# Kernel optimization log

Hardware: AMD Instinct MI355X
Metric: run time of the kernel (lower is better)

## Reference

```python
import jax, jax.numpy as jnp
import numpy as np

N_HEADS = 8

def lstm_step(x, h, c, W_ih, W_hh, b_ih, b_hh):
    # torch LSTMCell: gate order i, f, g, o
    gates = x @ W_ih.T + b_ih + h @ W_hh.T + b_hh
    i, f, g, o = jnp.split(gates, 4, axis=-1)
    c = jax.nn.sigmoid(f) * c + jax.nn.sigmoid(i) * jnp.tanh(g)
    h = jax.nn.sigmoid(o) * jnp.tanh(c)
    return h, c

def mha(query, key, value, attn_mask, Wq, bq, Wk, bk, Wv, bv, Wo, bo):
    # query [B,1,H], key/value [B,N,H], attn_mask [B,1,N] (True = masked)
    B, N, H = key.shape
    dh = H // N_HEADS
    q = (query @ Wq.T + bq).reshape(B, 1, N_HEADS, dh)
    k = (key @ Wk.T + bk).reshape(B, N, N_HEADS, dh)
    v = (value @ Wv.T + bv).reshape(B, N, N_HEADS, dh)
    scores = jnp.einsum('bqhd,bnhd->bhqn', q, k) / jnp.sqrt(jnp.asarray(dh, q.dtype))
    scores = jnp.where(attn_mask[:, None, :, :], jnp.asarray(-1e9, scores.dtype), scores)
    attn = jax.nn.softmax(scores, axis=-1)
    out = jnp.einsum('bhqn,bnhd->bqhd', attn, v).reshape(B, 1, H)
    return out @ Wo.T + bo

def setup_inputs() -> dict:
    B, S, V, E, G, HI, N = 32, 128, 32000, 512, 1024, 512, 16
    ks = jax.random.split(jax.random.key(0), 24)
    s = 0.05
    inp = {}
    inp['entity_feature'] = jax.random.normal(ks[0], (B, HI), jnp.float32)
    inp['neighbor_feature'] = jax.random.normal(ks[1], (B, N, HI), jnp.float32)
    inp['neighbor_num'] = jax.random.randint(ks[2], (B,), 1, N + 1)
    inp['img_feature'] = jax.random.normal(ks[3], (B, HI), jnp.float32)
    inp['target_sent'] = jax.random.randint(ks[4], (B, S), 0, V)
    inp['target_sent_len'] = jax.random.randint(ks[5], (B,), 1, S)
    emb = jax.random.normal(ks[6], (V, E), jnp.float32) * s
    inp['embedding'] = emb.at[0].set(0.0)  # padding_idx = 0
    inp['W_ih'] = jax.random.normal(ks[7], (4 * G, E), jnp.float32) * s
    inp['W_hh'] = jax.random.normal(ks[8], (4 * G, G), jnp.float32) * s
    inp['b_ih'] = jnp.zeros((4 * G,), jnp.float32)
    inp['b_hh'] = jnp.zeros((4 * G,), jnp.float32)
    inp['W_img'] = jax.random.normal(ks[9], (E, 3 * HI), jnp.float32) * s
    inp['b_img'] = jnp.zeros((E,), jnp.float32)
    inp['W_out'] = jax.random.normal(ks[10], (V, G), jnp.float32) * s
    inp['b_out'] = jnp.zeros((V,), jnp.float32)
    inp['Wq'] = jax.random.normal(ks[11], (HI, HI), jnp.float32) * s
    inp['bq'] = jnp.zeros((HI,), jnp.float32)
    inp['Wk'] = jax.random.normal(ks[12], (HI, HI), jnp.float32) * s
    inp['bk'] = jnp.zeros((HI,), jnp.float32)
    inp['Wv'] = jax.random.normal(ks[13], (HI, HI), jnp.float32) * s
    inp['bv'] = jnp.zeros((HI,), jnp.float32)
    inp['Wo'] = jax.random.normal(ks[14], (HI, HI), jnp.float32) * s
    inp['bo'] = jnp.zeros((HI,), jnp.float32)
    return inp

def reference(entity_feature, neighbor_feature, neighbor_num, img_feature,
              target_sent, target_sent_len, embedding,
              W_ih, W_hh, b_ih, b_hh, W_img, b_img, W_out, b_out,
              Wq, bq, Wk, bk, Wv, bv, Wo, bo):
    B = img_feature.shape[0]
    G = W_hh.shape[1]
    N = neighbor_feature.shape[1]
    # generate_final_feature: masked MHA of entity over neighbors
    mask = (neighbor_num[:, None] <= jnp.arange(N)[None, :])[:, None, :]  # [B,1,N]
    attn_out = mha(entity_feature[:, None, :], neighbor_feature, neighbor_feature, mask,
                   Wq, bq, Wk, bk, Wv, bv, Wo, bo).reshape(B, -1)
    final_feature = jnp.concatenate([entity_feature, attn_out, img_feature], axis=-1)
    img_embed = jnp.tanh(final_feature @ W_img.T + b_img)  # [B,E]
    z = jnp.zeros((B, G), img_embed.dtype)
    h, c = lstm_step(img_embed, z, z, W_ih, W_hh, b_ih, b_hh)
    # teacher forcing over t = 0..S-2 (dropout is identity in eval mode)
    x = embedding[target_sent[:, :-1]]  # [B, S-1, E]
    def step(carry, xt):
        h, c = carry
        h, c = lstm_step(xt, h, c, W_ih, W_hh, b_ih, b_hh)
        return (h, c), h @ W_out.T + b_out
    _, logits = jax.lax.scan(step, (h, c), jnp.swapaxes(x, 0, 1))  # [S-1,B,V]
    pred_words_probs = jnp.swapaxes(logits, 0, 1)  # [B, S-1, V]
    return pred_words_probs, target_sent, target_sent_len
```

## Files before the change

### kernel.cpp

```cpp
#include <hip/hip_runtime.h>
#include <math.h>

typedef short v8s __attribute__((ext_vector_type(8)));
typedef float v4f __attribute__((ext_vector_type(4)));

#define B_   32
#define S_   128
#define V_   32000
#define E_   512
#define G_   1024
#define HI_  512
#define NN_  16
#define NH_  8
#define DH_  64
#define TSTEPS 127
#define LOGN  4064000L
#define SCAN_BLOCKS 128

__device__ __forceinline__ short to_bf16(float x) {
  union { float f; unsigned u; } a; a.f = x;
  unsigned r = (a.u + 0x7FFFu + ((a.u >> 16) & 1u)) >> 16;
  return (short)r;
}
__device__ __forceinline__ float sigf(float x) { return 1.f / (1.f + expf(-x)); }

__device__ __forceinline__ void load_lds16(const void* g, void* l) {
  __builtin_amdgcn_global_load_lds((const __attribute__((address_space(1))) void*)g,
                                   (__attribute__((address_space(3))) void*)l, 16, 0, 0);
}

__global__ void prep_kernel(const float* __restrict__ Wih, const float* __restrict__ Whh,
                            const float* __restrict__ Wout, const float* __restrict__ bih,
                            const float* __restrict__ bhh, const int* __restrict__ sent,
                            const int* __restrict__ slen,
                            short* __restrict__ Wih_b, short* __restrict__ Whh_b,
                            short* __restrict__ Wout_b, float* __restrict__ bsum,
                            float* __restrict__ outTail, unsigned* __restrict__ flags) {
  const long nWo = 32768000L, nWh = 4194304L, nWi = 2097152L;
  const long NT = nWo + nWh + nWi + 4096 + 4096 + 32 + 128;
  long stride = (long)gridDim.x * blockDim.x;
  for (long i = (long)blockIdx.x * blockDim.x + threadIdx.x; i < NT; i += stride) {
    if (i < nWo) { Wout_b[i] = to_bf16(Wout[i]); continue; }
    long j = i - nWo;
    if (j < nWh) { Whh_b[j] = to_bf16(Whh[j]); continue; }
    j -= nWh;
    if (j < nWi) { Wih_b[j] = to_bf16(Wih[j]); continue; }
    j -= nWi;
    if (j < 4096) { bsum[j] = bih[j] + bhh[j]; continue; }
    j -= 4096;
    if (j < 4096) { outTail[j] = (float)sent[j]; continue; }
    j -= 4096;
    if (j < 32) { outTail[4096 + j] = (float)slen[j]; continue; }
    j -= 32;
    flags[j] = 0u;
  }
}

__global__ void dotk(const float* __restrict__ X, const float* __restrict__ W,
                     const float* __restrict__ bias, float* __restrict__ out,
                     int M, int N, int K, int act) {
  int o = blockIdx.x * 256 + threadIdx.x;
  if (o >= M * N) return;
  int m = o / N, n = o % N;
  const float4* x4 = (const float4*)(X + (long)m * K);
  const float4* w4 = (const float4*)(W + (long)n * K);
  float s = 0.f;
  int k4 = K >> 2;
  for (int k = 0; k < k4; ++k) {
    float4 a = x4[k], b = w4[k];
    s += a.x * b.x + a.y * b.y + a.z * b.z + a.w * b.w;
  }
  s += bias[n];
  if (act) s = tanhf(s);
  out[o] = s;
}

__global__ void attnk(const float* __restrict__ q, const float* __restrict__ k,
                      const float* __restrict__ v, const int* __restrict__ nnum,
                      float* __restrict__ ctx) {
  __shared__ float sc[NN_], at[NN_];
  int blk = blockIdx.x;
  int b = blk >> 3, h = blk & 7;
  int t = threadIdx.x;
  if (t < NN_) {
    const float* qp = q + b * HI_ + h * DH_;
    const float* kp = k + (long)(b * NN_ + t) * HI_ + h * DH_;
    float s = 0.f;
    for (int d = 0; d < DH_; ++d) s += qp[d] * kp[d];
    s *= 0.125f;
    if (t >= nnum[b]) s = -1e9f;
    sc[t] = s;
  }
  __syncthreads();
  if (t == 0) {
    float mx = sc[0];
    for (int n = 1; n < NN_; ++n) mx = fmaxf(mx, sc[n]);
    float sum = 0.f;
    for (int n = 0; n < NN_; ++n) { float e = expf(sc[n] - mx); at[n] = e; sum += e; }
    float inv = 1.f / sum;
    for (int n = 0; n < NN_; ++n) at[n] *= inv;
  }
  __syncthreads();
  float acc = 0.f;
  for (int n = 0; n < NN_; ++n)
    acc += at[n] * v[(long)(b * NN_ + n) * HI_ + h * DH_ + t];
  ctx[b * HI_ + h * DH_ + t] = acc;
}

__global__ void concatk(const float* __restrict__ ent, const float* __restrict__ ao,
                        const float* __restrict__ img, float* __restrict__ ff) {
  int i = blockIdx.x * 256 + threadIdx.x;
  if (i >= B_ * 3 * HI_) return;
  int b = i / (3 * HI_), j = i % (3 * HI_);
  float vv;
  if (j < HI_) vv = ent[b * HI_ + j];
  else if (j < 2 * HI_) vv = ao[b * HI_ + j - HI_];
  else vv = img[b * HI_ + j - 2 * HI_];
  ff[i] = vv;
}

__global__ void lstm0(const float* __restrict__ g0, float* __restrict__ c0,
                      short* __restrict__ HB) {
  int i = blockIdx.x * 256 + threadIdx.x;
  if (i >= B_ * G_) return;
  int b = i >> 10, u = i & 1023;
  const float* gr = g0 + (long)b * 4096;
  float ig = gr[u], gg = gr[2048 + u], og = gr[3072 + u];
  float c = sigf(ig) * tanhf(gg);
  float h = sigf(og) * tanhf(c);
  c0[i] = c;
  HB[i] = to_bf16(h);
}

__global__ void gatherk(const float* __restrict__ emb, const int* __restrict__ sent,
                        short* __restrict__ Xemb) {
  int i = blockIdx.x * 256 + threadIdx.x;
  if (i >= 4096 * 512) return;
  int mrow = i >> 9, e = i & 511;
  int t = mrow >> 5, b = mrow & 31;
  float vv = 0.f;
  if (t < TSTEPS) { int w = sent[b * S_ + t]; vv = emb[(long)w * E_ + e]; }
  Xemb[i] = to_bf16(vv);
}

__global__ __launch_bounds__(256) void gemm_bt(const short* __restrict__ A,
                                               const short* __restrict__ Bm,
                                               const float* __restrict__ bias,
                                               float* __restrict__ C,
                                               int M, int N, int K, int mode) {
  __shared__ short As[128 * 32];
  __shared__ short Bs[128 * 32];
  const int tid = threadIdx.x;
  const int lane = tid & 63, wave = tid >> 6;
  const int n0 = blockIdx.x * 128, m0 = blockIdx.y * 128;
  const int l15 = lane & 15, quad = lane >> 4;
  const int mhalf = wave & 1, nhalf = wave >> 1;
  const int srow = lane >> 2;
  const int sseg = (lane & 3) * 8;
  v4f acc[4][4];
#pragma unroll
  for (int i = 0; i < 4; i++)
#pragma unroll
    for (int j = 0; j < 4; j++) acc[i][j] = (v4f){0.f, 0.f, 0.f, 0.f};
  const int kiters = K >> 5;
  for (int kt = 0; kt < kiters; ++kt) {
    const int k0 = kt * 32;
#pragma unroll
    for (int c = 0; c < 2; ++c) {
      const int chunk = wave * 2 + c;
      const int row = chunk * 16 + srow;
      load_lds16(A + (long)(m0 + row) * K + k0 + sseg, &As[chunk * 512]);
      load_lds16(Bm + (long)(n0 + row) * K + k0 + sseg, &Bs[chunk * 512]);
    }
    __syncthreads();
    v8s af[4], wf[4];
#pragma unroll
    for (int i = 0; i < 4; i++) af[i] = *(const v8s*)&As[(mhalf * 64 + i * 16 + l15) * 32 + quad * 8];
#pragma unroll
    for (int j = 0; j < 4; j++) wf[j] = *(const v8s*)&Bs[(nhalf * 64 + j * 16 + l15) * 32 + quad * 8];
#pragma unroll
    for (int i = 0; i < 4; i++)
#pragma unroll
      for (int j = 0; j < 4; j++)
        acc[i][j] = __builtin_amdgcn_mfma_f32_16x16x32_bf16(af[i], wf[j], acc[i][j], 0, 0, 0);
    __syncthreads();
  }
#pragma unroll
  for (int i = 0; i < 4; i++) {
    const int mb = m0 + mhalf * 64 + i * 16 + quad * 4;
#pragma unroll
    for (int j = 0; j < 4; j++) {
      const int nc = n0 + nhalf * 64 + j * 16 + l15;
      const float bv = bias[nc];
#pragma unroll
      for (int r = 0; r < 4; r++) {
        const int m = mb + r;
        float vv = acc[i][j][r] + bv;
        if (mode == 0) {
          C[(long)m * N + nc] = vv;
        } else if (m >= 32) {
          const int b = m & 31, t = (m >> 5) - 1;
          C[(long)b * LOGN + (long)t * V_ + nc] = vv;
        }
      }
    }
  }
}

__global__ __launch_bounds__(256) void lstm_scan(const float* __restrict__ Xg,
                                                 const short* __restrict__ Whh_b,
                                                 const float* __restrict__ c0,
                                                 short* __restrict__ HB,
                                                 unsigned* __restrict__ flags) {
  __shared__ short Wl[32 * 1032];
  __shared__ short Hl[32 * 1032];
  __shared__ float gl[32 * 33];
  __shared__ float cl[256];
  const int tid = threadIdx.x, nb = blockIdx.x;
  const int lane = tid & 63, wave = tid >> 6;
  const int l15 = lane & 15, quad = lane >> 4;
  const int mt = wave & 1, nt = wave >> 1;

  for (int cid = tid; cid < 4096; cid += 256) {
    int lrow = cid >> 7;
    int koff = (cid & 127) * 8;
    int u = lrow >> 2, g = lrow & 3;
    const short* src = Whh_b + (long)(g * 1024 + nb * 8 + u) * 1024 + koff;
    *(v8s*)&Wl[lrow * 1032 + koff] = *(const v8s*)src;
  }
  const int eu = tid >> 5, eb = tid & 31, gu = nb * 8 + eu;
  cl[tid] = c0[eb * 1024 + gu];
  __syncthreads();

  float x0, x1, x2, x3;
  {
    const float* xr = Xg + (long)eb * 4096 + gu;
    x0 = xr[0]; x1 = xr[1024]; x2 = xr[2048]; x3 = xr[3072];
  }

  for (int tt = 0; tt < TSTEPS; ++tt) {
    {
      const short* hsrc = HB + (long)tt * 32 * 1024;
#pragma unroll
      for (int it = 0; it < 16; ++it) {
        int cid = it * 256 + tid;
        int row = cid >> 7;
        int koff = (cid & 127) * 8;
        *(v8s*)&Hl[row * 1032 + koff] = *(const v8s*)(hsrc + cid * 8);
      }
    }
    __syncthreads();
    v4f acc0 = (v4f){0.f, 0.f, 0.f, 0.f};
    v4f acc1 = (v4f){0.f, 0.f, 0.f, 0.f};
    {
      const short* aP = &Hl[(mt * 16 + l15) * 1032 + quad * 8];
      const short* wP = &Wl[(nt * 16 + l15) * 1032 + quad * 8];
#pragma unroll
      for (int kk = 0; kk < 32; kk += 2) {
        v8s a0 = *(const v8s*)(aP + kk * 32);
        v8s w0 = *(const v8s*)(wP + kk * 32);
        v8s a1 = *(const v8s*)(aP + (kk + 1) * 32);
        v8s w1 = *(const v8s*)(wP + (kk + 1) * 32);
        acc0 = __builtin_amdgcn_mfma_f32_16x16x32_bf16(a0, w0, acc0, 0, 0, 0);
        acc1 = __builtin_amdgcn_mfma_f32_16x16x32_bf16(a1, w1, acc1, 0, 0, 0);
      }
    }
#pragma unroll
    for (int r = 0; r < 4; ++r)
      gl[(nt * 16 + l15) * 33 + mt * 16 + quad * 4 + r] = acc0[r] + acc1[r];
    __syncthreads();
    float ig = gl[(eu * 4 + 0) * 33 + eb] + x0;
    float fg = gl[(eu * 4 + 1) * 33 + eb] + x1;
    float gg = gl[(eu * 4 + 2) * 33 + eb] + x2;
    float og = gl[(eu * 4 + 3) * 33 + eb] + x3;
    float c = sigf(fg) * cl[tid] + sigf(ig) * tanhf(gg);
    float h = sigf(og) * tanhf(c);
    cl[tid] = c;
    unsigned hb = (unsigned)(unsigned short)to_bf16(h);
    unsigned ob = (unsigned)__shfl((int)hb, lane ^ 32, 64);
    if ((lane & 32) == 0) {
      unsigned packed = hb | (ob << 16);
      unsigned* dst = (unsigned*)HB + ((long)(tt + 1) * 32 + eb) * 512 + nb * 4 + wave;
      __hip_atomic_store(dst, packed, __ATOMIC_RELAXED, __HIP_MEMORY_SCOPE_AGENT);
    }
    asm volatile("s_waitcnt vmcnt(0)" ::: "memory");
    __syncthreads();
    if (tt < TSTEPS - 1) {
      if (tid == 0)
        __hip_atomic_store(flags + nb, (unsigned)(tt + 1), __ATOMIC_RELAXED, __HIP_MEMORY_SCOPE_AGENT);
      {
        const float* xn = Xg + ((long)(tt + 1) * 32 + eb) * 4096 + gu;
        x0 = xn[0]; x1 = xn[1024]; x2 = xn[2048]; x3 = xn[3072];
      }
      if (tid < 64) {
        const unsigned long long* fp = (const unsigned long long*)flags + tid;
        const unsigned tgt = (unsigned)(tt + 1);
        for (;;) {
          unsigned long long v = __hip_atomic_load(fp, __ATOMIC_RELAXED, __HIP_MEMORY_SCOPE_AGENT);
          if ((unsigned)v >= tgt && (unsigned)(v >> 32) >= tgt) break;
          __builtin_amdgcn_s_sleep(2);
        }
      }
      __syncthreads();
    }
  }
}

extern "C" void kernel_launch(void* const* d_in, const int* in_sizes, int n_in,
                              void* d_out, int out_size, void* d_ws, size_t ws_size,
                              hipStream_t stream) {
  const float* ent  = (const float*)d_in[0];
  const float* nei  = (const float*)d_in[1];
  const int*   nnum = (const int*)d_in[2];
  const float* img  = (const float*)d_in[3];
  const int*   sent = (const int*)d_in[4];
  const int*   slen = (const int*)d_in[5];
  const float* emb  = (const float*)d_in[6];
  const float* Wih  = (const float*)d_in[7];
  const float* Whh  = (const float*)d_in[8];
  const float* bih  = (const float*)d_in[9];
  const float* bhh  = (const float*)d_in[10];
  const float* Wimg = (const float*)d_in[11];
  const float* bimg = (const float*)d_in[12];
  const float* Wout = (const float*)d_in[13];
  const float* bout = (const float*)d_in[14];
  const float* Wq = (const float*)d_in[15]; const float* bq = (const float*)d_in[16];
  const float* Wk = (const float*)d_in[17]; const float* bk = (const float*)d_in[18];
  const float* Wv = (const float*)d_in[19]; const float* bv = (const float*)d_in[20];
  const float* Wo = (const float*)d_in[21]; const float* bo = (const float*)d_in[22];
  float* out = (float*)d_out;

  char* ws = (char*)d_ws;
  short* Wout_b = (short*)(ws + 0L);
  short* Whh_b  = (short*)(ws + 65536000L);
  short* Wih_b  = (short*)(ws + 73924608L);
  float* bsum   = (float*)(ws + 78118912L);
  short* Xemb   = (short*)(ws + 78135296L);
  short* HB     = (short*)(ws + 82329600L);
  float* qbuf   = (float*)(ws + 90718208L);
  float* kbuf   = (float*)(ws + 90783744L);
  float* vbuf   = (float*)(ws + 91832320L);
  float* ctxb   = (float*)(ws + 92880896L);
  float* aob    = (float*)(ws + 92946432L);
  float* ffb    = (float*)(ws + 93011968L);
  float* ieb    = (float*)(ws + 93208576L);
  float* g0b    = (float*)(ws + 93274112L);
  float* c0b    = (float*)(ws + 93798400L);
  unsigned* flags = (unsigned*)(ws + 93929472L);
  float* Xg = out;
  float* outTail = out + (long)B_ * TSTEPS * V_;

  prep_kernel<<<16384, 256, 0, stream>>>(Wih, Whh, Wout, bih, bhh, sent, slen,
                                         Wih_b, Whh_b, Wout_b, bsum, outTail, flags);
  dotk<<<64, 256, 0, stream>>>(ent, Wq, bq, qbuf, 32, 512, 512, 0);
  dotk<<<1024, 256, 0, stream>>>(nei, Wk, bk, kbuf, 512, 512, 512, 0);
  dotk<<<1024, 256, 0, stream>>>(nei, Wv, bv, vbuf, 512, 512, 512, 0);
  attnk<<<256, 64, 0, stream>>>(qbuf, kbuf, vbuf, nnum, ctxb);
  dotk<<<64, 256, 0, stream>>>(ctxb, Wo, bo, aob, 32, 512, 512, 0);
  concatk<<<192, 256, 0, stream>>>(ent, aob, img, ffb);
  dotk<<<64, 256, 0, stream>>>(ffb, Wimg, bimg, ieb, 32, 512, 1536, 1);
  dotk<<<512, 256, 0, stream>>>(ieb, Wih, bsum, g0b, 32, 4096, 512, 0);
  lstm0<<<128, 256, 0, stream>>>(g0b, c0b, HB);
  gatherk<<<8192, 256, 0, stream>>>(emb, sent, Xemb);
  gemm_bt<<<dim3(32, 32), 256, 0, stream>>>(Xemb, Wih_b, bsum, Xg, 4096, 4096, 512, 0);
  lstm_scan<<<SCAN_BLOCKS, 256, 0, stream>>>(Xg, Whh_b, c0b, HB, flags);
  gemm_bt<<<dim3(250, 32), 256, 0, stream>>>(HB, Wout_b, bout, out, 4096, 32000, 1024, 1);
}
```

Baseline: 2.182 ms.

## Fuse vocab projection GEMM into LSTM scan as flag-gated worker blocks

The scan kernel now launches extra worker blocks that run the 4096x32000x1024 output GEMM tile by tile. Each worker spins on the per-block step flags until the hidden states its M-tile needs are published, so the projection overlaps the serial recurrence instead of running after it. The input-gate precompute is written into the output buffer in an interleaved layout, so each scan thread reads its four gates with one float4 load. Workers overwrite that scratch region only after the scan has consumed it. In exchange the GEMM gets half as many blocks, and correctness depends on all 256 blocks being co-resident and on the flag ordering.

```diff
diff --git a/kernel.cpp b/kernel.cpp
--- a/kernel.cpp
+++ b/kernel.cpp
@@ -16,6 +16,10 @@
 #define TSTEPS 127
 #define LOGN  4064000L
 #define SCAN_BLOCKS 128
+#define WORK_BLOCKS 128
+#define NTILES 250
+#define MTILES 32
+#define TOTTILES 8000
 
 __device__ __forceinline__ short to_bf16(float x) {
   union { float f; unsigned u; } a; a.f = x;
@@ -198,27 +202,132 @@
         float vv = acc[i][j][r] + bv;
         if (mode == 0) {
           C[(long)m * N + nc] = vv;
-        } else if (m >= 32) {
-          const int b = m & 31, t = (m >> 5) - 1;
-          C[(long)b * LOGN + (long)t * V_ + nc] = vv;
-        }
-      }
-    }
-  }
-}
-
-__global__ __launch_bounds__(256) void lstm_scan(const float* __restrict__ Xg,
-                                                 const short* __restrict__ Whh_b,
-                                                 const float* __restrict__ c0,
-                                                 short* __restrict__ HB,
-                                                 unsigned* __restrict__ flags) {
-  __shared__ short Wl[32 * 1032];
-  __shared__ short Hl[32 * 1032];
-  __shared__ float gl[32 * 33];
-  __shared__ float cl[256];
+        } else {
+          if (m < 4064) {
+            const int u = m >> 5, b = m & 31;
+            const int uu = nc & 1023, g = nc >> 10;
+            C[(long)b * LOGN + (long)u * 32000 + (uu >> 3) * 32 + (uu & 7) * 4 + g] = vv;
+          }
+        }
+      }
+    }
+  }
+}
+
+__global__ __launch_bounds__(256) void lstm_scan(const short* Whh_b,
+                                                 const float* c0,
+                                                 short* HB,
+                                                 unsigned* flags,
+                                                 const short* Wout_b,
+                                                 const float* bout,
+                                                 float* outb) {
+  __shared__ __align__(16) char smem[137344];
   const int tid = threadIdx.x, nb = blockIdx.x;
   const int lane = tid & 63, wave = tid >> 6;
   const int l15 = lane & 15, quad = lane >> 4;
+  const int mhalf = wave & 1, nhalf = wave >> 1;
+
+  if (nb >= SCAN_BLOCKS) {
+    const int wid = nb - SCAN_BLOCKS;
+    const int rsub = lane >> 3;
+    const int cswz = ((lane & 7) * 16) ^ (rsub << 4);
+    int lastm = -1;
+    for (int q = wid; q < TOTTILES; q += WORK_BLOCKS) {
+      const int mt_ = q / NTILES, nt_ = q % NTILES;
+      const int m0 = mt_ * 128, n0 = nt_ * 128;
+      if (mt_ != lastm) {
+        lastm = mt_;
+        unsigned tgt = (unsigned)(mt_ * 4 + 3);
+        if (tgt > 127u) tgt = 127u;
+        if (tid < 64) {
+          const unsigned long long* fp = (const unsigned long long*)flags + tid;
+          for (;;) {
+            unsigned long long vv = __hip_atomic_load(fp, __ATOMIC_RELAXED, __HIP_MEMORY_SCOPE_AGENT);
+            if ((unsigned)vv >= tgt && (unsigned)(vv >> 32) >= tgt) break;
+            __builtin_amdgcn_s_sleep(4);
+          }
+        }
+        asm volatile("" ::: "memory");
+        __syncthreads();
+      }
+      v4f acc[4][4];
+#pragma unroll
+      for (int i = 0; i < 4; i++)
+#pragma unroll
+        for (int j = 0; j < 4; j++) acc[i][j] = (v4f){0.f, 0.f, 0.f, 0.f};
+
+      auto wissue = [&](int s2) {
+        if (s2 < 16) {
+          const long k0b = (long)s2 * 128;
+          char* Ab = smem + (s2 & 3) * 32768;
+          char* Bb = Ab + 16384;
+#pragma unroll
+          for (int c = 0; c < 4; ++c) {
+            const int rowb = wave * 32 + c * 8;
+            load_lds16((const char*)HB + (long)(m0 + rowb + rsub) * 2048 + k0b + cswz,
+                       Ab + rowb * 128);
+            load_lds16((const char*)Wout_b + (long)(n0 + rowb + rsub) * 2048 + k0b + cswz,
+                       Bb + rowb * 128);
+          }
+        }
+      };
+      wissue(0); wissue(1); wissue(2);
+      for (int s = 0; s < 16; ++s) {
+        wissue(s + 3);
+        if (s <= 12)      asm volatile("s_waitcnt vmcnt(24)" ::: "memory");
+        else if (s == 13) asm volatile("s_waitcnt vmcnt(16)" ::: "memory");
+        else if (s == 14) asm volatile("s_waitcnt vmcnt(8)" ::: "memory");
+        else              asm volatile("s_waitcnt vmcnt(0)" ::: "memory");
+        __builtin_amdgcn_s_barrier();
+        const short* Ab = (const short*)(smem + (s & 3) * 32768);
+        const short* Bb = Ab + 8192;
+#pragma unroll
+        for (int kk = 0; kk < 2; ++kk) {
+          v8s af[4], bf[4];
+#pragma unroll
+          for (int i = 0; i < 4; ++i) {
+            const int row = mhalf * 64 + i * 16 + l15;
+            af[i] = *(const v8s*)(Ab + row * 64 + ((kk * 32 + quad * 8) ^ ((row & 7) << 3)));
+          }
+#pragma unroll
+          for (int j = 0; j < 4; ++j) {
+            const int row = nhalf * 64 + j * 16 + l15;
+            bf[j] = *(const v8s*)(Bb + row * 64 + ((kk * 32 + quad * 8) ^ ((row & 7) << 3)));
+          }
+#pragma unroll
+          for (int i = 0; i < 4; ++i)
+#pragma unroll
+            for (int j = 0; j < 4; ++j)
+              acc[i][j] = __builtin_amdgcn_mfma_f32_16x16x32_bf16(af[i], bf[j], acc[i][j], 0, 0, 0);
+        }
+        asm volatile("" ::: "memory");
+        __builtin_amdgcn_s_barrier();
+      }
+#pragma unroll
+      for (int i = 0; i < 4; i++) {
+        const int mb = m0 + mhalf * 64 + i * 16 + quad * 4;
+#pragma unroll
+        for (int j = 0; j < 4; j++) {
+          const int nc = n0 + nhalf * 64 + j * 16 + l15;
+          const float bv = bout[nc];
+#pragma unroll
+          for (int r = 0; r < 4; r++) {
+            const int m = mb + r;
+            if (m >= 32) {
+              const int b = m & 31, t = (m >> 5) - 1;
+              outb[(long)b * LOGN + (long)t * V_ + nc] = acc[i][j][r] + bv;
+            }
+          }
+        }
+      }
+    }
+    return;
+  }
+
+  short* Wl = (short*)smem;
+  short* Hl = (short*)(smem + 66048);
+  float* gl = (float*)(smem + 132096);
+  float* cl = (float*)(smem + 136320);
   const int mt = wave & 1, nt = wave >> 1;
 
   for (int cid = tid; cid < 4096; cid += 256) {
@@ -232,10 +341,10 @@
   cl[tid] = c0[eb * 1024 + gu];
   __syncthreads();
 
-  float x0, x1, x2, x3;
+  float4 xg4;
   {
-    const float* xr = Xg + (long)eb * 4096 + gu;
-    x0 = xr[0]; x1 = xr[1024]; x2 = xr[2048]; x3 = xr[3072];
+    const float4* xp = (const float4*)(outb + (long)eb * LOGN + (long)(nb * 32 + eu * 4));
+    xg4 = *xp;
   }
 
   for (int tt = 0; tt < TSTEPS; ++tt) {
@@ -269,10 +378,10 @@
     for (int r = 0; r < 4; ++r)
       gl[(nt * 16 + l15) * 33 + mt * 16 + quad * 4 + r] = acc0[r] + acc1[r];
     __syncthreads();
-    float ig = gl[(eu * 4 + 0) * 33 + eb] + x0;
-    float fg = gl[(eu * 4 + 1) * 33 + eb] + x1;
-    float gg = gl[(eu * 4 + 2) * 33 + eb] + x2;
-    float og = gl[(eu * 4 + 3) * 33 + eb] + x3;
+    float ig = gl[(eu * 4 + 0) * 33 + eb] + xg4.x;
+    float fg = gl[(eu * 4 + 1) * 33 + eb] + xg4.y;
+    float gg = gl[(eu * 4 + 2) * 33 + eb] + xg4.z;
+    float og = gl[(eu * 4 + 3) * 33 + eb] + xg4.w;
     float c = sigf(fg) * cl[tid] + sigf(ig) * tanhf(gg);
     float h = sigf(og) * tanhf(c);
     cl[tid] = c;
@@ -285,12 +394,13 @@
     }
     asm volatile("s_waitcnt vmcnt(0)" ::: "memory");
     __syncthreads();
+    if (tid == 0)
+      __hip_atomic_store(flags + nb, (unsigned)(tt + 1), __ATOMIC_RELAXED, __HIP_MEMORY_SCOPE_AGENT);
     if (tt < TSTEPS - 1) {
-      if (tid == 0)
-        __hip_atomic_store(flags + nb, (unsigned)(tt + 1), __ATOMIC_RELAXED, __HIP_MEMORY_SCOPE_AGENT);
       {
-        const float* xn = Xg + ((long)(tt + 1) * 32 + eb) * 4096 + gu;
-        x0 = xn[0]; x1 = xn[1024]; x2 = xn[2048]; x3 = xn[3072];
+        const float4* xp = (const float4*)(outb + (long)eb * LOGN +
+                                           (long)(tt + 1) * 32000 + (nb * 32 + eu * 4));
+        xg4 = *xp;
       }
       if (tid < 64) {
         const unsigned long long* fp = (const unsigned long long*)flags + tid;
@@ -347,7 +457,6 @@
   float* g0b    = (float*)(ws + 93274112L);
   float* c0b    = (float*)(ws + 93798400L);
   unsigned* flags = (unsigned*)(ws + 93929472L);
-  float* Xg = out;
   float* outTail = out + (long)B_ * TSTEPS * V_;
 
   prep_kernel<<<16384, 256, 0, stream>>>(Wih, Whh, Wout, bih, bhh, sent, slen,
@@ -362,7 +471,7 @@
   dotk<<<512, 256, 0, stream>>>(ieb, Wih, bsum, g0b, 32, 4096, 512, 0);
   lstm0<<<128, 256, 0, stream>>>(g0b, c0b, HB);
   gatherk<<<8192, 256, 0, stream>>>(emb, sent, Xemb);
-  gemm_bt<<<dim3(32, 32), 256, 0, stream>>>(Xemb, Wih_b, bsum, Xg, 4096, 4096, 512, 0);
-  lstm_scan<<<SCAN_BLOCKS, 256, 0, stream>>>(Xg, Whh_b, c0b, HB, flags);
-  gemm_bt<<<dim3(250, 32), 256, 0, stream>>>(HB, Wout_b, bout, out, 4096, 32000, 1024, 1);
-}
+  gemm_bt<<<dim3(32, 32), 256, 0, stream>>>(Xemb, Wih_b, bsum, out, 4096, 4096, 512, 2);
+  lstm_scan<<<SCAN_BLOCKS + WORK_BLOCKS, 256, 0, stream>>>(Whh_b, c0b, HB, flags,
+                                                           Wout_b, bout, out);
+}
```

Result: no change. 2.211 ms (+1.3%).
